# Kernel tuning notes

Measured on AMD Instinct MI355X. Metric: run time of the kernel, lower is better.

The kernel has to match this reference:

```python
import jax, jax.numpy as jnp
import numpy as np

D_I = 1024
D_O = 1024
B = 4
S = 4096

def setup_inputs() -> dict:
    key = jax.random.key(0)
    kx, kq, kk, kv = jax.random.split(key, 4)
    x = jax.random.normal(kx, (B, S, D_I), dtype=jnp.float32)
    # torch Linear(d_i, d_o) weight is [d_o, d_i]; we store transposed [d_i, d_o]
    sc = 1.0 / np.sqrt(D_I)
    Wq = jax.random.uniform(kq, (D_I, D_O), jnp.float32, -sc, sc)
    Wk = jax.random.uniform(kk, (D_I, D_O), jnp.float32, -sc, sc)
    Wv = jax.random.uniform(kv, (D_I, D_O), jnp.float32, -sc, sc)
    return {"x": x, "Wq": Wq, "Wk": Wk, "Wv": Wv}

def reference(x, Wq, Wk, Wv):
    # x: [B, S, d_i]
    q = jnp.einsum('bsd,de->bse', x, Wq)  # [B,S,d_o]
    k = jnp.einsum('bsd,de->bse', x, Wk)
    v = jnp.einsum('bsd,de->bse', x, Wv)
    scores = jnp.einsum('bqe,bke->bqk', q, k)  # [B,S,S]
    S_len = x.shape[1]
    causal = jnp.tril(jnp.ones((S_len, S_len), dtype=bool))  # keep lower tri
    scores = jnp.where(causal[None], scores, -jnp.inf)
    attn = jax.nn.softmax(scores / jnp.sqrt(jnp.float32(v.shape[-1])), axis=-1)
    # dropout p=0.0 -> identity
    return jnp.einsum('bqk,bke->bqe', attn, v)  # [B,S,d_o]
```

## Files before the change

kernel.cpp:

```cpp
#include <hip/hip_runtime.h>

typedef __bf16 bf16x8 __attribute__((ext_vector_type(8)));
typedef float f32x4 __attribute__((ext_vector_type(4)));

#define B_SZ 4
#define S_SZ 4096
#define D_SZ 1024
#define ELEMS_MAT ((size_t)B_SZ * S_SZ * D_SZ)

#define OFF_Q  ((size_t)0)
#define OFF_K  (ELEMS_MAT)
#define OFF_VT (2 * ELEMS_MAT)
#define ZONE   (3 * ELEMS_MAT)
#define OFF_XB (ZONE)
#define OFF_WT (ZONE + 2 * ELEMS_MAT)
#define OFF_S  (ZONE)
#define S_BATCH ((size_t)8912896)
#define OFF_LP (ZONE + 4 * S_BATCH)

#define MFMA16(a, b, c) __builtin_amdgcn_mfma_f32_16x16x32_bf16((a), (b), (c), 0, 0, 0)

static __device__ __forceinline__ unsigned short f2bf(float f) {
  __bf16 h = (__bf16)f;
  return __builtin_bit_cast(unsigned short, h);
}
static __device__ __forceinline__ float Ef(float x) {
  return __builtin_exp2f(x * 1.44269504f);
}

static __device__ __forceinline__ void async_lds16(const void* g, void* l) {
  __builtin_amdgcn_global_load_lds((__attribute__((address_space(1))) void*)g,
                                   (__attribute__((address_space(3))) void*)l, 16, 0, 0);
}

__global__ void cast_x_kernel(const float* __restrict__ x, unsigned short* __restrict__ xb) {
  size_t i = ((size_t)blockIdx.x * 256 + threadIdx.x) * 8;
  f32x4 a = *(const f32x4*)(x + i);
  f32x4 b = *(const f32x4*)(x + i + 4);
  bf16x8 o;
  o[0] = (__bf16)a[0]; o[1] = (__bf16)a[1]; o[2] = (__bf16)a[2]; o[3] = (__bf16)a[3];
  o[4] = (__bf16)b[0]; o[5] = (__bf16)b[1]; o[6] = (__bf16)b[2]; o[7] = (__bf16)b[3];
  *(bf16x8*)(xb + i) = o;
}

__global__ void cast_wt_kernel(const float* __restrict__ Wq, const float* __restrict__ Wk,
                               const float* __restrict__ Wv, unsigned short* __restrict__ Wt) {
  __shared__ float tl[64][65];
  const float* W = blockIdx.z == 0 ? Wq : (blockIdx.z == 1 ? Wk : Wv);
  unsigned short* out = Wt + (size_t)blockIdx.z * (size_t)D_SZ * (size_t)D_SZ;
  const int k0 = blockIdx.x * 64, n0 = blockIdx.y * 64;
  const int t = threadIdx.x;
  for (int i = t; i < 4096; i += 256) {
    int r = i >> 6, c = i & 63;
    tl[r][c] = W[(size_t)(k0 + r) * D_SZ + n0 + c];
  }
  __syncthreads();
  for (int i = t; i < 4096; i += 256) {
    int r = i >> 6, c = i & 63;
    out[(size_t)(n0 + r) * D_SZ + k0 + c] = f2bf(tl[c][r]);
  }
}

static __device__ __forceinline__ bf16x8 lds_frag(const char* half, int r, int hi) {
  return *(const bf16x8*)(half + r * 64 + ((hi * 16) ^ (((r >> 1) & 3) << 4)));
}

static __device__ __forceinline__ void stage_half256(const char* src, size_t ld, char* lds, int tid) {
#pragma unroll
  for (int it = 0; it < 2; ++it) {
    int i = it * 512 + tid;
    int row = i >> 2;
    int s = (i & 3) ^ ((row >> 1) & 3);
    async_lds16(src + (size_t)row * ld + s * 16, lds + i * 16);
  }
}
static __device__ __forceinline__ void stage_half128(const char* src, size_t ld, char* lds, int tid) {
  int row = tid >> 2;
  int s = (tid & 3) ^ ((row >> 1) & 3);
  async_lds16(src + (size_t)row * ld + s * 16, lds + tid * 16);
}

static __device__ __forceinline__ void mainloop8p(const char* A, size_t lda,
                                                  const char* B, size_t ldb, int NT,
                                                  char sm[2][2][2][16384],
                                                  int tid, f32x4 acc[8][4]) {
  const int lane = tid & 63, w = tid >> 6;
  const int wm = w >> 2, wn = w & 3, lr = lane & 15, hi = lane >> 4;
  stage_half256(A,      lda, sm[0][0][0], tid);
  stage_half256(B,      ldb, sm[0][1][0], tid);
  stage_half256(A + 64, lda, sm[0][0][1], tid);
  stage_half256(B + 64, ldb, sm[0][1][1], tid);
  asm volatile("s_waitcnt vmcnt(4)" ::: "memory");
  __builtin_amdgcn_s_barrier();
  for (int t = 0; t < NT; ++t) {
    const int d = t & 1;
    const char* At1 = A + (size_t)(t + 1) * 128;
    const char* Bt1 = B + (size_t)(t + 1) * 128;
    const bool pre = (t + 1 < NT);
    bf16x8 af[4], bfr[4];
#pragma unroll
    for (int g = 0; g < 4; ++g) bfr[g] = lds_frag(sm[d][1][0], wn * 64 + g * 16 + lr, hi);
#pragma unroll
    for (int f = 0; f < 4; ++f) af[f] = lds_frag(sm[d][0][0], wm * 128 + f * 16 + lr, hi);
    if (pre) stage_half256(At1, lda, sm[d ^ 1][0][0], tid);
    __builtin_amdgcn_s_barrier();
    asm volatile("s_waitcnt lgkmcnt(0)" ::: "memory");
    __builtin_amdgcn_s_setprio(1);
#pragma unroll
    for (int f = 0; f < 4; ++f)
#pragma unroll
      for (int g = 0; g < 4; ++g) acc[f][g] = MFMA16(af[f], bfr[g], acc[f][g]);
    __builtin_amdgcn_s_setprio(0);
    __builtin_amdgcn_s_barrier();
#pragma unroll
    for (int f = 0; f < 4; ++f) af[f] = lds_frag(sm[d][0][0], wm * 128 + 64 + f * 16 + lr, hi);
    if (pre) stage_half256(Bt1, ldb, sm[d ^ 1][1][0], tid);
    __builtin_amdgcn_s_barrier();
    asm volatile("s_waitcnt lgkmcnt(0)" ::: "memory");
    __builtin_amdgcn_s_setprio(1);
#pragma unroll
    for (int f = 0; f < 4; ++f)
#pragma unroll
      for (int g = 0; g < 4; ++g) acc[4 + f][g] = MFMA16(af[f], bfr[g], acc[4 + f][g]);
    __builtin_amdgcn_s_setprio(0);
    if (pre) asm volatile("s_waitcnt vmcnt(4)" ::: "memory");
    else     asm volatile("s_waitcnt vmcnt(0)" ::: "memory");
    __builtin_amdgcn_s_barrier();
#pragma unroll
    for (int g = 0; g < 4; ++g) bfr[g] = lds_frag(sm[d][1][1], wn * 64 + g * 16 + lr, hi);
#pragma unroll
    for (int f = 0; f < 4; ++f) af[f] = lds_frag(sm[d][0][1], wm * 128 + f * 16 + lr, hi);
    if (pre) stage_half256(At1 + 64, lda, sm[d ^ 1][0][1], tid);
    __builtin_amdgcn_s_barrier();
    asm volatile("s_waitcnt lgkmcnt(0)" ::: "memory");
    __builtin_amdgcn_s_setprio(1);
#pragma unroll
    for (int f = 0; f < 4; ++f)
#pragma unroll
      for (int g = 0; g < 4; ++g) acc[f][g] = MFMA16(af[f], bfr[g], acc[f][g]);
    __builtin_amdgcn_s_setprio(0);
    __builtin_amdgcn_s_barrier();
#pragma unroll
    for (int f = 0; f < 4; ++f) af[f] = lds_frag(sm[d][0][1], wm * 128 + 64 + f * 16 + lr, hi);
    if (pre) stage_half256(Bt1 + 64, ldb, sm[d ^ 1][1][1], tid);
    __builtin_amdgcn_s_barrier();
    asm volatile("s_waitcnt lgkmcnt(0)" ::: "memory");
    __builtin_amdgcn_s_setprio(1);
#pragma unroll
    for (int f = 0; f < 4; ++f)
#pragma unroll
      for (int g = 0; g < 4; ++g) acc[4 + f][g] = MFMA16(af[f], bfr[g], acc[4 + f][g]);
    __builtin_amdgcn_s_setprio(0);
    if (pre) asm volatile("s_waitcnt vmcnt(4)" ::: "memory");
    __builtin_amdgcn_s_barrier();
  }
}

#define GEMM_PRE()                                    \
  __shared__ char sm[2][2][2][16384];                 \
  const int tid = threadIdx.x;                        \
  f32x4 acc[8][4];                                    \
  {                                                   \
    const f32x4 z4 = {0.f, 0.f, 0.f, 0.f};            \
    _Pragma("unroll") for (int f = 0; f < 8; ++f)     \
      _Pragma("unroll") for (int g = 0; g < 4; ++g)   \
        acc[f][g] = z4;                               \
  }

#define EPI_IDX()                                     \
  const int lane = tid & 63, w = tid >> 6;            \
  const int wm = w >> 2, wn = w & 3;                  \
  const int lr = lane & 15, hi = lane >> 4;

__global__ __launch_bounds__(512, 2) void gemm_qkv256(const unsigned short* __restrict__ xb,
                                                      const unsigned short* __restrict__ Wt,
                                                      unsigned short* __restrict__ Q,
                                                      unsigned short* __restrict__ K,
                                                      unsigned short* __restrict__ Vt) {
  GEMM_PRE();
  const int bid = blockIdx.x;
  const int sw = (bid & 7) * 96 + (bid >> 3);
  const int mt = sw % 64, nt = sw / 64;
  const char* A = (const char*)xb + (size_t)mt * 256 * 2048;
  const char* Bp = (const char*)Wt + (size_t)nt * 256 * 2048;
  mainloop8p(A, 2048, Bp, 2048, 16, sm, tid, acc);
  EPI_IDX();
  if (nt < 8) {
    unsigned short* Out = (nt >> 2) == 0 ? Q : K;
    const int nb = (nt & 3) * 256;
#pragma unroll
    for (int f = 0; f < 8; ++f)
#pragma unroll
      for (int g = 0; g < 4; ++g)
#pragma unroll
        for (int j = 0; j < 4; ++j) {
          const int m = mt * 256 + wm * 128 + f * 16 + hi * 4 + j;
          const int n = nb + wn * 64 + g * 16 + lr;
          Out[(size_t)m * D_SZ + n] = f2bf(acc[f][g][j]);
        }
  } else {
#pragma unroll
    for (int f = 0; f < 8; ++f)
#pragma unroll
      for (int g = 0; g < 4; ++g) {
        const int m = mt * 256 + wm * 128 + f * 16 + hi * 4;
        const int n = (nt - 8) * 256 + wn * 64 + g * 16 + lr;
        const int b = m >> 12, s = m & 4095;
        ushort4 pk;
        pk.x = f2bf(acc[f][g][0]); pk.y = f2bf(acc[f][g][1]);
        pk.z = f2bf(acc[f][g][2]); pk.w = f2bf(acc[f][g][3]);
        *(ushort4*)(Vt + (size_t)b * (D_SZ * S_SZ) + (size_t)n * S_SZ + s) = pk;
      }
  }
}

__global__ __launch_bounds__(512, 2) void s_gemm256(const unsigned short* __restrict__ Q,
                                                    const unsigned short* __restrict__ K,
                                                    unsigned short* __restrict__ Sp,
                                                    float* __restrict__ lp) {
  GEMM_PRE();
  const int bid = blockIdx.x;
  const int sw = (bid & 7) * 68 + (bid >> 3);
  const int b = sw / 136;
  const int tile = sw % 136;
  int I = (int)((sqrtf(8.0f * tile + 1.0f) - 1.0f) * 0.5f);
  while ((I + 1) * (I + 2) / 2 <= tile) ++I;
  while (I * (I + 1) / 2 > tile) --I;
  const int J = tile - I * (I + 1) / 2;
  const char* A = (const char*)Q + ((size_t)b * S_SZ + (size_t)I * 256) * 2048;
  const char* Bp = (const char*)K + ((size_t)b * S_SZ + (size_t)J * 256) * 2048;
  mainloop8p(A, 2048, Bp, 2048, 16, sm, tid, acc);
  EPI_IDX();
  const int L = (I + 1) * 256;
  unsigned short* So = Sp + (size_t)b * S_BATCH + (size_t)(I * (I + 1) / 2) * 65536;
  float* shl = (float*)sm;
  __syncthreads();
#pragma unroll
  for (int f = 0; f < 8; ++f) {
#pragma unroll
    for (int j = 0; j < 4; ++j) {
      const int m = wm * 128 + f * 16 + hi * 4 + j;
      float se = 0.f;
#pragma unroll
      for (int g = 0; g < 4; ++g) {
        const int n = J * 256 + wn * 64 + g * 16 + lr;
        float v = acc[f][g][j] * 0.03125f;
        if (n > I * 256 + m) v = -1e30f;
        float ev = Ef(v);
        So[(size_t)m * L + n] = f2bf(ev);
        se += ev;
      }
      se += __shfl_xor(se, 1);
      se += __shfl_xor(se, 2);
      se += __shfl_xor(se, 4);
      se += __shfl_xor(se, 8);
      if (lr == 0) shl[wn * 256 + m] = se;
    }
  }
  __syncthreads();
  if (tid < 256) {
    float ll = shl[tid] + shl[256 + tid] + shl[512 + tid] + shl[768 + tid];
    lp[J * 16384 + b * 4096 + I * 256 + tid] = ll;
  }
}

__global__ __launch_bounds__(256) void sum_stats(float* __restrict__ lp) {
  const int r = blockIdx.x * 256 + threadIdx.x;
  const int I = (r & 4095) >> 8;
  float l = 0.f;
  for (int J = 0; J <= I; ++J) l += lp[J * 16384 + r];
  lp[r] = 1.0f / l;
}

static __device__ __forceinline__ void mainloop2p128(const char* A, size_t lda,
                                                     const char* B, size_t ldb, int NT,
                                                     char smA[2][2][16384],
                                                     char smB[2][2][8192],
                                                     int tid, f32x4 acc[4][4]) {
  const int lane = tid & 63, w = tid >> 6;
  const int wm = w >> 1, wn = w & 1, lr = lane & 15, hi = lane >> 4;
  stage_half256(A,      lda, smA[0][0], tid);
  stage_half128(B,      ldb, smB[0][0], tid);
  stage_half256(A + 64, lda, smA[0][1], tid);
  stage_half128(B + 64, ldb, smB[0][1], tid);
  asm volatile("s_waitcnt vmcnt(3)" ::: "memory");
  __builtin_amdgcn_s_barrier();
  for (int t = 0; t < NT; ++t) {
    const int d = t & 1;
    const char* At1 = A + (size_t)(t + 1) * 128;
    const char* Bt1 = B + (size_t)(t + 1) * 128;
    const bool pre = (t + 1 < NT);
    bf16x8 af[4], bfr[4];
#pragma unroll
    for (int g = 0; g < 4; ++g) bfr[g] = lds_frag(smB[d][0], wn * 64 + g * 16 + lr, hi);
#pragma unroll
    for (int f = 0; f < 4; ++f) af[f] = lds_frag(smA[d][0], wm * 64 + f * 16 + lr, hi);
    if (pre) { stage_half256(At1, lda, smA[d ^ 1][0], tid); stage_half128(Bt1, ldb, smB[d ^ 1][0], tid); }
    __builtin_amdgcn_s_barrier();
    asm volatile("s_waitcnt lgkmcnt(0)" ::: "memory");
    __builtin_amdgcn_s_setprio(1);
#pragma unroll
    for (int f = 0; f < 4; ++f)
#pragma unroll
      for (int g = 0; g < 4; ++g) acc[f][g] = MFMA16(af[f], bfr[g], acc[f][g]);
    __builtin_amdgcn_s_setprio(0);
    if (pre) asm volatile("s_waitcnt vmcnt(3)" ::: "memory");
    else     asm volatile("s_waitcnt vmcnt(0)" ::: "memory");
    __builtin_amdgcn_s_barrier();
#pragma unroll
    for (int g = 0; g < 4; ++g) bfr[g] = lds_frag(smB[d][1], wn * 64 + g * 16 + lr, hi);
#pragma unroll
    for (int f = 0; f < 4; ++f) af[f] = lds_frag(smA[d][1], wm * 64 + f * 16 + lr, hi);
    if (pre) { stage_half256(At1 + 64, lda, smA[d ^ 1][1], tid); stage_half128(Bt1 + 64, ldb, smB[d ^ 1][1], tid); }
    __builtin_amdgcn_s_barrier();
    asm volatile("s_waitcnt lgkmcnt(0)" ::: "memory");
    __builtin_amdgcn_s_setprio(1);
#pragma unroll
    for (int f = 0; f < 4; ++f)
#pragma unroll
      for (int g = 0; g < 4; ++g) acc[f][g] = MFMA16(af[f], bfr[g], acc[f][g]);
    __builtin_amdgcn_s_setprio(0);
    if (pre) asm volatile("s_waitcnt vmcnt(3)" ::: "memory");
    __builtin_amdgcn_s_barrier();
  }
}

__global__ __launch_bounds__(512, 2) void pv_bal(const unsigned short* __restrict__ Sp,
                                                 const unsigned short* __restrict__ Vt,
                                                 const float* __restrict__ lp,
                                                 float* __restrict__ out) {
  __shared__ char smA[2][2][16384];
  __shared__ char smB[2][2][8192];
  const int tid = threadIdx.x;
  const int bid = blockIdx.x;
  const int sw = (bid & 7) * 32 + (bid >> 3);
  const int p = sw >> 5, b = (sw >> 3) & 3, nt = sw & 7;
  const int lane = tid & 63, w = tid >> 6;
  const int wm = w >> 1, wn = w & 1;
  const int lr = lane & 15, hi = lane >> 4;
  f32x4 acc[4][4];
#pragma unroll
  for (int half = 0; half < 2; ++half) {
    const int I = half ? (15 - p) : p;
    {
      const f32x4 z4 = {0.f, 0.f, 0.f, 0.f};
#pragma unroll
      for (int f = 0; f < 4; ++f)
#pragma unroll
        for (int g = 0; g < 4; ++g) acc[f][g] = z4;
    }
    const char* A = (const char*)(Sp + (size_t)b * S_BATCH + (size_t)(I * (I + 1) / 2) * 65536);
    const size_t lda = (size_t)(I + 1) * 512;
    const char* Bp = (const char*)Vt + ((size_t)b * D_SZ + (size_t)nt * 128) * (S_SZ * 2);
    mainloop2p128(A, lda, Bp, S_SZ * 2, (I + 1) * 4, smA, smB, tid, acc);
#pragma unroll
    for (int f = 0; f < 4; ++f)
#pragma unroll
      for (int j = 0; j < 4; ++j) {
        const int m = wm * 64 + f * 16 + hi * 4 + j;
        const float rl = lp[b * 4096 + I * 256 + m];
#pragma unroll
        for (int g = 0; g < 4; ++g) {
          const int n = nt * 128 + wn * 64 + g * 16 + lr;
          out[((size_t)b * S_SZ + (size_t)I * 256 + m) * D_SZ + n] = acc[f][g][j] * rl;
        }
      }
    __syncthreads();
  }
}

extern "C" void kernel_launch(void* const* d_in, const int* in_sizes, int n_in,
                              void* d_out, int out_size, void* d_ws, size_t ws_size,
                              hipStream_t stream) {
  (void)in_sizes; (void)n_in; (void)out_size; (void)ws_size;
  const float* x  = (const float*)d_in[0];
  const float* Wq = (const float*)d_in[1];
  const float* Wk = (const float*)d_in[2];
  const float* Wv = (const float*)d_in[3];
  float* out = (float*)d_out;
  unsigned short* ws = (unsigned short*)d_ws;
  float* lp = (float*)(ws + OFF_LP);

  cast_x_kernel<<<8192, 256, 0, stream>>>(x, ws + OFF_XB);
  cast_wt_kernel<<<dim3(16, 16, 3), 256, 0, stream>>>(Wq, Wk, Wv, ws + OFF_WT);
  gemm_qkv256<<<768, 512, 0, stream>>>(ws + OFF_XB, ws + OFF_WT,
                                       ws + OFF_Q, ws + OFF_K, ws + OFF_VT);
  s_gemm256<<<544, 512, 0, stream>>>(ws + OFF_Q, ws + OFF_K, ws + OFF_S, lp);
  sum_stats<<<64, 256, 0, stream>>>(lp);
  pv_bal<<<256, 512, 0, stream>>>(ws + OFF_S, ws + OFF_VT, lp, out);
}
```

Baseline: 367.2 us.

## Split tail S tiles into half-width blocks and remap QKV tile order

After: 342.4 us (median of 2 runs). -6.7%, faster.

```diff
diff --git a/kernel.cpp b/kernel.cpp
--- a/kernel.cpp
+++ b/kernel.cpp
@@ -154,122 +154,6 @@
     if (pre) asm volatile("s_waitcnt vmcnt(4)" ::: "memory");
     __builtin_amdgcn_s_barrier();
   }
-}
-
-#define GEMM_PRE()                                    \
-  __shared__ char sm[2][2][2][16384];                 \
-  const int tid = threadIdx.x;                        \
-  f32x4 acc[8][4];                                    \
-  {                                                   \
-    const f32x4 z4 = {0.f, 0.f, 0.f, 0.f};            \
-    _Pragma("unroll") for (int f = 0; f < 8; ++f)     \
-      _Pragma("unroll") for (int g = 0; g < 4; ++g)   \
-        acc[f][g] = z4;                               \
-  }
-
-#define EPI_IDX()                                     \
-  const int lane = tid & 63, w = tid >> 6;            \
-  const int wm = w >> 2, wn = w & 3;                  \
-  const int lr = lane & 15, hi = lane >> 4;
-
-__global__ __launch_bounds__(512, 2) void gemm_qkv256(const unsigned short* __restrict__ xb,
-                                                      const unsigned short* __restrict__ Wt,
-                                                      unsigned short* __restrict__ Q,
-                                                      unsigned short* __restrict__ K,
-                                                      unsigned short* __restrict__ Vt) {
-  GEMM_PRE();
-  const int bid = blockIdx.x;
-  const int sw = (bid & 7) * 96 + (bid >> 3);
-  const int mt = sw % 64, nt = sw / 64;
-  const char* A = (const char*)xb + (size_t)mt * 256 * 2048;
-  const char* Bp = (const char*)Wt + (size_t)nt * 256 * 2048;
-  mainloop8p(A, 2048, Bp, 2048, 16, sm, tid, acc);
-  EPI_IDX();
-  if (nt < 8) {
-    unsigned short* Out = (nt >> 2) == 0 ? Q : K;
-    const int nb = (nt & 3) * 256;
-#pragma unroll
-    for (int f = 0; f < 8; ++f)
-#pragma unroll
-      for (int g = 0; g < 4; ++g)
-#pragma unroll
-        for (int j = 0; j < 4; ++j) {
-          const int m = mt * 256 + wm * 128 + f * 16 + hi * 4 + j;
-          const int n = nb + wn * 64 + g * 16 + lr;
-          Out[(size_t)m * D_SZ + n] = f2bf(acc[f][g][j]);
-        }
-  } else {
-#pragma unroll
-    for (int f = 0; f < 8; ++f)
-#pragma unroll
-      for (int g = 0; g < 4; ++g) {
-        const int m = mt * 256 + wm * 128 + f * 16 + hi * 4;
-        const int n = (nt - 8) * 256 + wn * 64 + g * 16 + lr;
-        const int b = m >> 12, s = m & 4095;
-        ushort4 pk;
-        pk.x = f2bf(acc[f][g][0]); pk.y = f2bf(acc[f][g][1]);
-        pk.z = f2bf(acc[f][g][2]); pk.w = f2bf(acc[f][g][3]);
-        *(ushort4*)(Vt + (size_t)b * (D_SZ * S_SZ) + (size_t)n * S_SZ + s) = pk;
-      }
-  }
-}
-
-__global__ __launch_bounds__(512, 2) void s_gemm256(const unsigned short* __restrict__ Q,
-                                                    const unsigned short* __restrict__ K,
-                                                    unsigned short* __restrict__ Sp,
-                                                    float* __restrict__ lp) {
-  GEMM_PRE();
-  const int bid = blockIdx.x;
-  const int sw = (bid & 7) * 68 + (bid >> 3);
-  const int b = sw / 136;
-  const int tile = sw % 136;
-  int I = (int)((sqrtf(8.0f * tile + 1.0f) - 1.0f) * 0.5f);
-  while ((I + 1) * (I + 2) / 2 <= tile) ++I;
-  while (I * (I + 1) / 2 > tile) --I;
-  const int J = tile - I * (I + 1) / 2;
-  const char* A = (const char*)Q + ((size_t)b * S_SZ + (size_t)I * 256) * 2048;
-  const char* Bp = (const char*)K + ((size_t)b * S_SZ + (size_t)J * 256) * 2048;
-  mainloop8p(A, 2048, Bp, 2048, 16, sm, tid, acc);
-  EPI_IDX();
-  const int L = (I + 1) * 256;
-  unsigned short* So = Sp + (size_t)b * S_BATCH + (size_t)(I * (I + 1) / 2) * 65536;
-  float* shl = (float*)sm;
-  __syncthreads();
-#pragma unroll
-  for (int f = 0; f < 8; ++f) {
-#pragma unroll
-    for (int j = 0; j < 4; ++j) {
-      const int m = wm * 128 + f * 16 + hi * 4 + j;
-      float se = 0.f;
-#pragma unroll
-      for (int g = 0; g < 4; ++g) {
-        const int n = J * 256 + wn * 64 + g * 16 + lr;
-        float v = acc[f][g][j] * 0.03125f;
-        if (n > I * 256 + m) v = -1e30f;
-        float ev = Ef(v);
-        So[(size_t)m * L + n] = f2bf(ev);
-        se += ev;
-      }
-      se += __shfl_xor(se, 1);
-      se += __shfl_xor(se, 2);
-      se += __shfl_xor(se, 4);
-      se += __shfl_xor(se, 8);
-      if (lr == 0) shl[wn * 256 + m] = se;
-    }
-  }
-  __syncthreads();
-  if (tid < 256) {
-    float ll = shl[tid] + shl[256 + tid] + shl[512 + tid] + shl[768 + tid];
-    lp[J * 16384 + b * 4096 + I * 256 + tid] = ll;
-  }
-}
-
-__global__ __launch_bounds__(256) void sum_stats(float* __restrict__ lp) {
-  const int r = blockIdx.x * 256 + threadIdx.x;
-  const int I = (r & 4095) >> 8;
-  float l = 0.f;
-  for (int J = 0; J <= I; ++J) l += lp[J * 16384 + r];
-  lp[r] = 1.0f / l;
 }
 
 static __device__ __forceinline__ void mainloop2p128(const char* A, size_t lda,
@@ -325,6 +209,189 @@
   }
 }
 
+__global__ __launch_bounds__(512, 2) void gemm_qkv256(const unsigned short* __restrict__ xb,
+                                                      const unsigned short* __restrict__ Wt,
+                                                      unsigned short* __restrict__ Q,
+                                                      unsigned short* __restrict__ K,
+                                                      unsigned short* __restrict__ Vt) {
+  __shared__ char sm[2][2][2][16384];
+  const int tid = threadIdx.x;
+  f32x4 acc[8][4];
+  {
+    const f32x4 z4 = {0.f, 0.f, 0.f, 0.f};
+#pragma unroll
+    for (int f = 0; f < 8; ++f)
+#pragma unroll
+      for (int g = 0; g < 4; ++g) acc[f][g] = z4;
+  }
+  const int bid = blockIdx.x;
+  const int sw = (bid & 7) * 96 + (bid >> 3);
+  const int mt = sw / 12, nt = sw % 12;
+  const char* A = (const char*)xb + (size_t)mt * 256 * 2048;
+  const char* Bp = (const char*)Wt + (size_t)nt * 256 * 2048;
+  mainloop8p(A, 2048, Bp, 2048, 16, sm, tid, acc);
+  const int lane = tid & 63, w = tid >> 6;
+  const int wm = w >> 2, wn = w & 3;
+  const int lr = lane & 15, hi = lane >> 4;
+  if (nt < 8) {
+    unsigned short* Out = (nt >> 2) == 0 ? Q : K;
+    const int nb = (nt & 3) * 256;
+#pragma unroll
+    for (int f = 0; f < 8; ++f)
+#pragma unroll
+      for (int g = 0; g < 4; ++g)
+#pragma unroll
+        for (int j = 0; j < 4; ++j) {
+          const int m = mt * 256 + wm * 128 + f * 16 + hi * 4 + j;
+          const int n = nb + wn * 64 + g * 16 + lr;
+          Out[(size_t)m * D_SZ + n] = f2bf(acc[f][g][j]);
+        }
+  } else {
+#pragma unroll
+    for (int f = 0; f < 8; ++f)
+#pragma unroll
+      for (int g = 0; g < 4; ++g) {
+        const int m = mt * 256 + wm * 128 + f * 16 + hi * 4;
+        const int n = (nt - 8) * 256 + wn * 64 + g * 16 + lr;
+        const int b = m >> 12, s = m & 4095;
+        ushort4 pk;
+        pk.x = f2bf(acc[f][g][0]); pk.y = f2bf(acc[f][g][1]);
+        pk.z = f2bf(acc[f][g][2]); pk.w = f2bf(acc[f][g][3]);
+        *(ushort4*)(Vt + (size_t)b * (D_SZ * S_SZ) + (size_t)n * S_SZ + s) = pk;
+      }
+  }
+}
+
+__global__ __launch_bounds__(512, 2) void s_gemm_mixed(const unsigned short* __restrict__ Q,
+                                                       const unsigned short* __restrict__ K,
+                                                       unsigned short* __restrict__ Sp,
+                                                       float* __restrict__ lp) {
+  __shared__ char sm[2][2][2][16384];
+  const int tid = threadIdx.x;
+  const int bid = blockIdx.x;
+  const int lane = tid & 63, w = tid >> 6;
+  const int lr = lane & 15, hi = lane >> 4;
+
+  if (bid < 64) {
+    char (*smA)[2][16384] = (char (*)[2][16384])sm;
+    char (*smB)[2][8192]  = (char (*)[2][8192])((char*)sm + 65536);
+    const int hid = (bid & 7) * 8 + (bid >> 3);
+    const int t = 104 + (hid >> 1);
+    const int parity = hid & 1;
+    int I = 13;
+    while ((I + 1) * (I + 2) / 2 <= t) ++I;
+    const int J = t - I * (I + 1) / 2;
+    const int Jh = 2 * J + parity;
+    const int b = 3;
+    f32x4 acc[4][4];
+    {
+      const f32x4 z4 = {0.f, 0.f, 0.f, 0.f};
+#pragma unroll
+      for (int f = 0; f < 4; ++f)
+#pragma unroll
+        for (int g = 0; g < 4; ++g) acc[f][g] = z4;
+    }
+    const char* A = (const char*)Q + ((size_t)b * S_SZ + (size_t)I * 256) * 2048;
+    const char* Bp = (const char*)K + ((size_t)b * S_SZ + (size_t)Jh * 128) * 2048;
+    mainloop2p128(A, 2048, Bp, 2048, 16, smA, smB, tid, acc);
+    const int wm = w >> 1, wn = w & 1;
+    const int L = (I + 1) * 256;
+    unsigned short* So = Sp + (size_t)b * S_BATCH + (size_t)(I * (I + 1) / 2) * 65536;
+    float* shl = (float*)smB;
+    __syncthreads();
+#pragma unroll
+    for (int f = 0; f < 4; ++f) {
+#pragma unroll
+      for (int j = 0; j < 4; ++j) {
+        const int m = wm * 64 + f * 16 + hi * 4 + j;
+        float se = 0.f;
+#pragma unroll
+        for (int g = 0; g < 4; ++g) {
+          const int nG = Jh * 128 + wn * 64 + g * 16 + lr;
+          float v = acc[f][g][j] * 0.03125f;
+          if (nG > I * 256 + m) v = -1e30f;
+          float ev = Ef(v);
+          So[(size_t)m * L + nG] = f2bf(ev);
+          se += ev;
+        }
+        se += __shfl_xor(se, 1);
+        se += __shfl_xor(se, 2);
+        se += __shfl_xor(se, 4);
+        se += __shfl_xor(se, 8);
+        if (lr == 0) shl[wn * 256 + m] = se;
+      }
+    }
+    __syncthreads();
+    if (tid < 256) {
+      float ll = shl[tid] + shl[256 + tid];
+      const int r = b * 4096 + I * 256 + tid;
+      if (parity == 0) lp[J * 16384 + r] = ll;
+      else atomicAdd(lp + 16 * 16384 + r, ll);
+    }
+  } else {
+    f32x4 acc[8][4];
+    {
+      const f32x4 z4 = {0.f, 0.f, 0.f, 0.f};
+#pragma unroll
+      for (int f = 0; f < 8; ++f)
+#pragma unroll
+        for (int g = 0; g < 4; ++g) acc[f][g] = z4;
+    }
+    const int fid = bid - 64;
+    const int sw = (fid & 7) * 64 + (fid >> 3);
+    const int b = sw / 136;
+    const int tile = sw % 136;
+    int I = (int)((sqrtf(8.0f * tile + 1.0f) - 1.0f) * 0.5f);
+    while ((I + 1) * (I + 2) / 2 <= tile) ++I;
+    while (I * (I + 1) / 2 > tile) --I;
+    const int J = tile - I * (I + 1) / 2;
+    const char* A = (const char*)Q + ((size_t)b * S_SZ + (size_t)I * 256) * 2048;
+    const char* Bp = (const char*)K + ((size_t)b * S_SZ + (size_t)J * 256) * 2048;
+    mainloop8p(A, 2048, Bp, 2048, 16, sm, tid, acc);
+    const int wm = w >> 2, wn = w & 3;
+    const int L = (I + 1) * 256;
+    unsigned short* So = Sp + (size_t)b * S_BATCH + (size_t)(I * (I + 1) / 2) * 65536;
+    float* shl = (float*)sm;
+    __syncthreads();
+#pragma unroll
+    for (int f = 0; f < 8; ++f) {
+#pragma unroll
+      for (int j = 0; j < 4; ++j) {
+        const int m = wm * 128 + f * 16 + hi * 4 + j;
+        float se = 0.f;
+#pragma unroll
+        for (int g = 0; g < 4; ++g) {
+          const int n = J * 256 + wn * 64 + g * 16 + lr;
+          float v = acc[f][g][j] * 0.03125f;
+          if (n > I * 256 + m) v = -1e30f;
+          float ev = Ef(v);
+          So[(size_t)m * L + n] = f2bf(ev);
+          se += ev;
+        }
+        se += __shfl_xor(se, 1);
+        se += __shfl_xor(se, 2);
+        se += __shfl_xor(se, 4);
+        se += __shfl_xor(se, 8);
+        if (lr == 0) shl[wn * 256 + m] = se;
+      }
+    }
+    __syncthreads();
+    if (tid < 256) {
+      float ll = shl[tid] + shl[256 + tid] + shl[512 + tid] + shl[768 + tid];
+      lp[J * 16384 + b * 4096 + I * 256 + tid] = ll;
+    }
+  }
+}
+
+__global__ __launch_bounds__(256) void sum_stats(float* __restrict__ lp) {
+  const int r = blockIdx.x * 256 + threadIdx.x;
+  const int I = (r & 4095) >> 8;
+  float l = 0.f;
+  for (int J = 0; J <= I; ++J) l += lp[J * 16384 + r];
+  if (r >= 15616) l += lp[16 * 16384 + r];
+  lp[r] = 1.0f / l;
+}
+
 __global__ __launch_bounds__(512, 2) void pv_bal(const unsigned short* __restrict__ Sp,
                                                  const unsigned short* __restrict__ Vt,
                                                  const float* __restrict__ lp,
@@ -385,7 +452,8 @@
   cast_wt_kernel<<<dim3(16, 16, 3), 256, 0, stream>>>(Wq, Wk, Wv, ws + OFF_WT);
   gemm_qkv256<<<768, 512, 0, stream>>>(ws + OFF_XB, ws + OFF_WT,
                                        ws + OFF_Q, ws + OFF_K, ws + OFF_VT);
-  s_gemm256<<<544, 512, 0, stream>>>(ws + OFF_Q, ws + OFF_K, ws + OFF_S, lp);
+  hipMemsetAsync(lp + 16 * 16384, 0, 16384 * sizeof(float), stream);
+  s_gemm_mixed<<<576, 512, 0, stream>>>(ws + OFF_Q, ws + OFF_K, ws + OFF_S, lp);
   sum_stats<<<64, 256, 0, stream>>>(lp);
   pv_bal<<<256, 512, 0, stream>>>(ws + OFF_S, ws + OFF_VT, lp, out);
 }
```
